# Kernel optimization log

Measured on AMD Instinct MI355X. Metric: run time of the kernel, lower is better.

## Reference

```python
import jax, jax.numpy as jnp
import numpy as np

N, D, K = 65536, 4096, 16
LN_EPS = 1e-5
SN_EPS = 1e-12
MIN_NORM = 1e-15


def setup_inputs() -> dict:
    key = jax.random.key(0)
    k1, k2, k3, k4 = jax.random.split(key, 4)
    return {
        "x": jax.random.normal(k1, (N, D), dtype=jnp.float32),
        "gamma": jnp.ones((D,), dtype=jnp.float32),
        "beta": jnp.zeros((D,), dtype=jnp.float32),
        "W": jax.random.normal(k2, (K, D), dtype=jnp.float32) * 0.02,
        "u": jax.random.normal(k3, (K,), dtype=jnp.float32),
        "log_scale": jnp.float32(-2.0),
    }


def _l2_normalize(v, eps=SN_EPS):
    return v / (jnp.linalg.norm(v) + eps)


def reference(x, gamma, beta, W, u, log_scale):
    # LayerNorm over last dim
    mean = jnp.mean(x, axis=-1, keepdims=True)
    var = jnp.mean(jnp.square(x - mean), axis=-1, keepdims=True)
    xn = (x - mean) * jax.lax.rsqrt(var + LN_EPS) * gamma + beta

    # spectral norm of W: one power iteration (torch spectral_norm forward)
    v = _l2_normalize(W.T @ u)           # [D]
    u_new = _l2_normalize(W @ v)         # [K]
    sigma = u_new @ (W @ v)              # scalar, top singular value estimate
    W_sn = W / sigma

    # linear (no bias) + learned scale
    vout = xn @ W_sn.T                   # [N, K]
    scale = jax.nn.sigmoid(log_scale) * 0.5
    vout = vout * scale

    # Poincare ball expmap0 with c=1: tanh(||v||) * v / ||v||
    vnorm = jnp.maximum(jnp.linalg.norm(vout, axis=-1, keepdims=True), MIN_NORM)
    return jnp.tanh(vnorm) * vout / vnorm
```

## Files before the change

kernel.cpp:

```cpp
#include <hip/hip_runtime.h>
#include <hip/hip_bf16.h>


#define ND 4096
#define NK 16
#define NROWS 65536

using f32x4  = __attribute__((ext_vector_type(4))) float;
using bf16x8 = __attribute__((ext_vector_type(8))) short;

#define GWB_OFF  0u
#define PART_OFF 131072u

__device__ __forceinline__ unsigned short f2bf(float f) {
    union { __hip_bfloat16 h; unsigned short u; } cv;
    cv.h = __float2bfloat16(f);
    return cv.u;
}

__global__ __launch_bounds__(256) void prep(
    const float* __restrict__ W, const float* __restrict__ gamma,
    const float* __restrict__ beta, const float* __restrict__ u,
    unsigned short* __restrict__ ws_gwb, float* __restrict__ ws_part)
{
    const int tid = threadIdx.x;
    const int d = blockIdx.x * 256 + tid;
    const int lane = tid & 63, wid = tid >> 6;

    float uu[NK];
#pragma unroll
    for (int k = 0; k < NK; ++k) uu[k] = u[k];
    const float g = gamma[d], b = beta[d];
    float w[NK];
#pragma unroll
    for (int k = 0; k < NK; ++k) w[k] = W[k * ND + d];

    float t = 0.f;
#pragma unroll
    for (int k = 0; k < NK; ++k) t = fmaf(w[k], uu[k], t);

    const int s  = d >> 5;
    const int wq = d & 31;
    const int lc = (wq >> 2) & 3;
    const int j  = (wq & 3) | ((wq >> 4) << 2);
    const int base = s * 512 + lc * 128 + j;

    float P[49];
#pragma unroll
    for (int k = 0; k < NK; ++k) {
        const float gw = g * w[k];
        ws_gwb[base + k * 8] = f2bf(gw);
        P[k]      = gw;
        P[16 + k] = b * w[k];
        P[32 + k] = w[k] * t;
    }
    P[48] = t * t;

#pragma unroll
    for (int m = 1; m < 64; m <<= 1) {
#pragma unroll
        for (int v = 0; v < 49; ++v) P[v] += __shfl_xor(P[v], m);
    }
    __shared__ float wred[4][49];
    if (lane == 0) {
#pragma unroll
        for (int v = 0; v < 49; ++v) wred[wid][v] = P[v];
    }
    __syncthreads();
    if (tid < 49)
        ws_part[blockIdx.x * 49 + tid] =
            (wred[0][tid] + wred[1][tid]) + (wred[2][tid] + wred[3][tid]);
}

__global__ __launch_bounds__(256, 8) void hyp_main(
    const float* __restrict__ x, const unsigned short* __restrict__ gwb_g,
    const float* __restrict__ ws_part, const float* __restrict__ log_scale,
    float* __restrict__ out)
{
    __shared__ float scl[49];

    const int tid  = threadIdx.x;
    const int lane = tid & 63;
    const int wid  = tid >> 6;
    const int tile = (blockIdx.x << 2) + wid;
    const int lr = lane & 15;
    const int lc = lane >> 4;

    const float* xp = x + (size_t)(tile * 16 + lr) * ND + lc * 4;
    const unsigned short* bp = gwb_g + lane * 8;
    const int start = (tile * 53) & 127;

    const f32x4 xa0 = *(const f32x4*)(xp + start * 32);
    const f32x4 xb0 = *(const f32x4*)(xp + start * 32 + 16);
    const bf16x8 bf0 = *(const bf16x8*)(bp + start * 512);

    if (tid < 49) {
        float s = 0.f;
#pragma unroll
        for (int b = 0; b < 16; ++b) s += ws_part[b * 49 + tid];
        scl[tid] = s;
    }
    __syncthreads();

    float ns2 = 0.f;
#pragma unroll
    for (int k = 0; k < NK; ++k) ns2 += scl[32 + k] * scl[32 + k];
    const float nt   = sqrtf(scl[48]) + 1e-12f;
    const float nwv  = sqrtf(ns2) / nt;
    const float sigma = (nwv * nwv) / (nwv + 1e-12f);
    const float coef = (0.5f / (1.0f + expf(-log_scale[0]))) / sigma;
    const float gk = scl[lr];
    const float bk = scl[16 + lr];

    f32x4 acc = {0.f, 0.f, 0.f, 0.f};
    float s1 = 0.f, s2 = 0.f;

#define PROC_BODY(XA, XB, BF) do {                                        \
        bf16x8 afrag;                                                     \
        afrag[0] = (short)f2bf(XA[0]); afrag[1] = (short)f2bf(XA[1]);     \
        afrag[2] = (short)f2bf(XA[2]); afrag[3] = (short)f2bf(XA[3]);     \
        afrag[4] = (short)f2bf(XB[0]); afrag[5] = (short)f2bf(XB[1]);     \
        afrag[6] = (short)f2bf(XB[2]); afrag[7] = (short)f2bf(XB[3]);     \
        s1 += ((XA[0] + XA[1]) + (XA[2] + XA[3]))                         \
            + ((XB[0] + XB[1]) + (XB[2] + XB[3]));                        \
        s2 = fmaf(XA[0], XA[0], s2); s2 = fmaf(XA[1], XA[1], s2);         \
        s2 = fmaf(XA[2], XA[2], s2); s2 = fmaf(XA[3], XA[3], s2);         \
        s2 = fmaf(XB[0], XB[0], s2); s2 = fmaf(XB[1], XB[1], s2);         \
        s2 = fmaf(XB[2], XB[2], s2); s2 = fmaf(XB[3], XB[3], s2);         \
        acc = __builtin_amdgcn_mfma_f32_16x16x32_bf16(afrag, (BF), acc, 0, 0, 0); \
    } while (0)

#define PROCESS(SS) do {                                                  \
        f32x4 xa = *(const f32x4*)(xp + (SS) * 32);                       \
        f32x4 xb = *(const f32x4*)(xp + (SS) * 32 + 16);                  \
        bf16x8 bfr = *(const bf16x8*)(bp + (SS) * 512);                   \
        PROC_BODY(xa, xb, bfr);                                           \
    } while (0)

    PROC_BODY(xa0, xb0, bf0);
#pragma unroll 2
    for (int s = start + 1; s < 128; ++s) PROCESS(s);
#pragma unroll 2
    for (int s = 0; s < start; ++s) PROCESS(s);
#undef PROCESS
#undef PROC_BODY

    s1 += __shfl_xor(s1, 16); s1 += __shfl_xor(s1, 32);
    s2 += __shfl_xor(s2, 16); s2 += __shfl_xor(s2, 32);
    const float mean = s1 * (1.0f / ND);
    const float var  = s2 * (1.0f / ND) - mean * mean;
    const float rstd = rsqrtf(var + 1e-5f);

    float vout[4];
#pragma unroll
    for (int j = 0; j < 4; ++j) {
        const int r = lc * 4 + j;
        const float m_r  = __shfl(mean, r);
        const float rs_r = __shfl(rstd, r);
        vout[j] = coef * (fmaf(-m_r, gk, acc[j]) * rs_r + bk);
    }

    float nsq[4];
#pragma unroll
    for (int j = 0; j < 4; ++j) nsq[j] = vout[j] * vout[j];
#pragma unroll
    for (int m = 1; m < 16; m <<= 1) {
#pragma unroll
        for (int j = 0; j < 4; ++j) nsq[j] += __shfl_xor(nsq[j], m);
    }

#pragma unroll
    for (int j = 0; j < 4; ++j) {
        float nv = sqrtf(nsq[j]);
        nv = fmaxf(nv, 1e-15f);
        const float fac = tanhf(nv) / nv;
        out[(size_t)(tile * 16 + lc * 4 + j) * NK + lr] = vout[j] * fac;
    }
}

extern "C" void kernel_launch(void* const* d_in, const int* in_sizes, int n_in,
                              void* d_out, int out_size, void* d_ws, size_t ws_size,
                              hipStream_t stream) {
    const float* x     = (const float*)d_in[0];
    const float* gamma = (const float*)d_in[1];
    const float* beta  = (const float*)d_in[2];
    const float* W     = (const float*)d_in[3];
    const float* u     = (const float*)d_in[4];
    const float* ls    = (const float*)d_in[5];

    char* ws = (char*)d_ws;
    unsigned short* ws_gwb = (unsigned short*)(ws + GWB_OFF);
    float* ws_part = (float*)(ws + PART_OFF);
    float* out     = (float*)d_out;

    prep<<<16, 256, 0, stream>>>(W, gamma, beta, u, ws_gwb, ws_part);
    hyp_main<<<1024, 256, 0, stream>>>(x, ws_gwb, ws_part, ls, out);
}
```

Baseline: 188.2 us.

## Fuse prep into main kernel with atomic-flag grid synchronization

Merges the weight-prep kernel into the main kernel. The first 16 blocks compute the bf16 gamma*W fragments and the partial sums, then bump a global counter with release semantics. Every block spins on that counter before reading the partials and the B fragments. This removes one kernel launch and the gap between kernels, but it adds a memset, a spin-wait that relies on blocks 0-15 being scheduled, and a launch-bounds occupancy hint lowered from 8 to 4.

After: 321.7 us. +70.9%, slower.

```diff
diff --git a/kernel.cpp b/kernel.cpp
--- a/kernel.cpp
+++ b/kernel.cpp
@@ -11,6 +11,7 @@
 
 #define GWB_OFF  0u
 #define PART_OFF 131072u
+#define FLAG_OFF 134208u
 
 __device__ __forceinline__ unsigned short f2bf(float f) {
     union { __hip_bfloat16 h; unsigned short u; } cv;
@@ -18,66 +19,15 @@
     return cv.u;
 }
 
-__global__ __launch_bounds__(256) void prep(
-    const float* __restrict__ W, const float* __restrict__ gamma,
-    const float* __restrict__ beta, const float* __restrict__ u,
-    unsigned short* __restrict__ ws_gwb, float* __restrict__ ws_part)
-{
-    const int tid = threadIdx.x;
-    const int d = blockIdx.x * 256 + tid;
-    const int lane = tid & 63, wid = tid >> 6;
-
-    float uu[NK];
-#pragma unroll
-    for (int k = 0; k < NK; ++k) uu[k] = u[k];
-    const float g = gamma[d], b = beta[d];
-    float w[NK];
-#pragma unroll
-    for (int k = 0; k < NK; ++k) w[k] = W[k * ND + d];
-
-    float t = 0.f;
-#pragma unroll
-    for (int k = 0; k < NK; ++k) t = fmaf(w[k], uu[k], t);
-
-    const int s  = d >> 5;
-    const int wq = d & 31;
-    const int lc = (wq >> 2) & 3;
-    const int j  = (wq & 3) | ((wq >> 4) << 2);
-    const int base = s * 512 + lc * 128 + j;
-
-    float P[49];
-#pragma unroll
-    for (int k = 0; k < NK; ++k) {
-        const float gw = g * w[k];
-        ws_gwb[base + k * 8] = f2bf(gw);
-        P[k]      = gw;
-        P[16 + k] = b * w[k];
-        P[32 + k] = w[k] * t;
-    }
-    P[48] = t * t;
-
-#pragma unroll
-    for (int m = 1; m < 64; m <<= 1) {
-#pragma unroll
-        for (int v = 0; v < 49; ++v) P[v] += __shfl_xor(P[v], m);
-    }
-    __shared__ float wred[4][49];
-    if (lane == 0) {
-#pragma unroll
-        for (int v = 0; v < 49; ++v) wred[wid][v] = P[v];
-    }
-    __syncthreads();
-    if (tid < 49)
-        ws_part[blockIdx.x * 49 + tid] =
-            (wred[0][tid] + wred[1][tid]) + (wred[2][tid] + wred[3][tid]);
-}
-
-__global__ __launch_bounds__(256, 8) void hyp_main(
-    const float* __restrict__ x, const unsigned short* __restrict__ gwb_g,
-    const float* __restrict__ ws_part, const float* __restrict__ log_scale,
-    float* __restrict__ out)
+__global__ __launch_bounds__(256, 4) void hyp_all(
+    const float* __restrict__ x, const float* __restrict__ W,
+    const float* __restrict__ gamma, const float* __restrict__ beta,
+    const float* __restrict__ u, const float* __restrict__ log_scale,
+    unsigned short* __restrict__ ws_gwb, float* __restrict__ ws_part,
+    unsigned int* __restrict__ flag, float* __restrict__ out)
 {
     __shared__ float scl[49];
+    __shared__ float wred[4][49];
 
     const int tid  = threadIdx.x;
     const int lane = tid & 63;
@@ -87,17 +37,76 @@
     const int lc = lane >> 4;
 
     const float* xp = x + (size_t)(tile * 16 + lr) * ND + lc * 4;
-    const unsigned short* bp = gwb_g + lane * 8;
+    const unsigned short* bp = ws_gwb + lane * 8;
     const int start = (tile * 53) & 127;
 
     const f32x4 xa0 = *(const f32x4*)(xp + start * 32);
     const f32x4 xb0 = *(const f32x4*)(xp + start * 32 + 16);
-    const bf16x8 bf0 = *(const bf16x8*)(bp + start * 512);
+
+    if (blockIdx.x < 16) {
+        const int d = (blockIdx.x << 8) + tid;
+        const float g = gamma[d], b = beta[d];
+        float w[NK];
+#pragma unroll
+        for (int k = 0; k < NK; ++k) w[k] = W[k * ND + d];
+        float t = 0.f;
+#pragma unroll
+        for (int k = 0; k < NK; ++k) t = fmaf(w[k], u[k], t);
+
+        const int wq  = d & 31;
+        const int base = (d >> 5) * 512 + ((wq >> 2) & 3) * 128
+                       + ((wq & 3) | ((wq >> 4) << 2));
+#pragma unroll
+        for (int k = 0; k < NK; ++k) ws_gwb[base + k * 8] = f2bf(g * w[k]);
+
+#define WRED16(EXPR, OFF) do {                                            \
+            float c[NK];                                                  \
+            _Pragma("unroll")                                             \
+            for (int k = 0; k < NK; ++k) c[k] = (EXPR);                   \
+            _Pragma("unroll")                                             \
+            for (int m = 1; m < 64; m <<= 1) {                            \
+                _Pragma("unroll")                                         \
+                for (int k = 0; k < NK; ++k) c[k] += __shfl_xor(c[k], m); \
+            }                                                             \
+            if (lane == 0) {                                              \
+                _Pragma("unroll")                                         \
+                for (int k = 0; k < NK; ++k) wred[wid][(OFF) + k] = c[k]; \
+            }                                                             \
+        } while (0)
+
+        WRED16(g * w[k], 0);
+        WRED16(b * w[k], 16);
+        WRED16(w[k] * t, 32);
+#undef WRED16
+        {
+            float c2 = t * t;
+#pragma unroll
+            for (int m = 1; m < 64; m <<= 1) c2 += __shfl_xor(c2, m);
+            if (lane == 0) wred[wid][48] = c2;
+        }
+        __syncthreads();
+        if (tid < 49)
+            ws_part[blockIdx.x * 49 + tid] =
+                (wred[0][tid] + wred[1][tid]) + (wred[2][tid] + wred[3][tid]);
+        __syncthreads();
+        if (tid == 0) {
+            __threadfence();
+            __hip_atomic_fetch_add(flag, 1u, __ATOMIC_RELEASE,
+                                   __HIP_MEMORY_SCOPE_AGENT);
+        }
+    }
+
+    if (lane == 0) {
+        while (__hip_atomic_load(flag, __ATOMIC_ACQUIRE,
+                                 __HIP_MEMORY_SCOPE_AGENT) < 16u)
+            __builtin_amdgcn_s_sleep(8);
+    }
+    __syncthreads();
 
     if (tid < 49) {
         float s = 0.f;
 #pragma unroll
-        for (int b = 0; b < 16; ++b) s += ws_part[b * 49 + tid];
+        for (int b2 = 0; b2 < 16; ++b2) s += ws_part[b2 * 49 + tid];
         scl[tid] = s;
     }
     __syncthreads();
@@ -137,7 +146,10 @@
         PROC_BODY(xa, xb, bfr);                                           \
     } while (0)
 
-    PROC_BODY(xa0, xb0, bf0);
+    {
+        const bf16x8 bf0 = *(const bf16x8*)(bp + start * 512);
+        PROC_BODY(xa0, xb0, bf0);
+    }
 #pragma unroll 2
     for (int s = start + 1; s < 128; ++s) PROCESS(s);
 #pragma unroll 2
@@ -191,8 +203,10 @@
     char* ws = (char*)d_ws;
     unsigned short* ws_gwb = (unsigned short*)(ws + GWB_OFF);
     float* ws_part = (float*)(ws + PART_OFF);
+    unsigned int* flag = (unsigned int*)(ws + FLAG_OFF);
     float* out     = (float*)d_out;
 
-    prep<<<16, 256, 0, stream>>>(W, gamma, beta, u, ws_gwb, ws_part);
-    hyp_main<<<1024, 256, 0, stream>>>(x, ws_gwb, ws_part, ls, out);
+    hipMemsetAsync(flag, 0, sizeof(unsigned int), stream);
+    hyp_all<<<1024, 256, 0, stream>>>(x, W, gamma, beta, u, ls,
+                                      ws_gwb, ws_part, flag, out);
 }
```
